# Performance work log

Measured on AMD Instinct MI355X. Metric: run time of the kernel, lower is better.

Reference implementation:

```python
import jax, jax.numpy as jnp
import numpy as np

N_NODES = 65536
N_GRAPHS = 32
NODES_PER_GRAPH = 2048
N_EDGES = 1048576
F_IN, H1, H2, OUT = 16, 64, 64, 12


def gcn_conv(x, src, dst, W, b, num_nodes):
    """PyG GCNConv: out = D^{-1/2} (A+I) D^{-1/2} X W + b."""
    loop = jnp.arange(num_nodes, dtype=src.dtype)
    s = jnp.concatenate([src, loop])  # sources incl. self-loops
    d = jnp.concatenate([dst, loop])  # targets incl. self-loops
    deg = jax.ops.segment_sum(jnp.ones_like(d, dtype=x.dtype), d, num_segments=num_nodes)
    dinv = jnp.where(deg > 0, jax.lax.rsqrt(deg), 0.0)
    norm = dinv[s] * dinv[d]  # [E+N]
    h = x @ W  # [N, H]
    msg = h[s] * norm[:, None]  # [E+N, H] -- dominant memory traffic
    return jax.ops.segment_sum(msg, d, num_segments=num_nodes) + b


def setup_inputs() -> dict:
    key = jax.random.key(0)
    k = jax.random.split(key, 8)
    x = jax.random.normal(k[0], (N_NODES, F_IN), dtype=jnp.float32)
    edge_index = jax.random.randint(k[1], (2, N_EDGES), 0, N_NODES, dtype=jnp.int32)
    batch = jnp.repeat(jnp.arange(N_GRAPHS, dtype=jnp.int32), NODES_PER_GRAPH)
    s1 = 1.0 / np.sqrt(F_IN)
    s2 = 1.0 / np.sqrt(H1)
    s3 = 1.0 / np.sqrt(H2 * NODES_PER_GRAPH)
    W1 = jax.random.uniform(k[2], (F_IN, H1), jnp.float32, -s1, s1)
    b1 = jnp.zeros((H1,), jnp.float32)
    W2 = jax.random.uniform(k[3], (H1, H2), jnp.float32, -s2, s2)
    b2 = jnp.zeros((H2,), jnp.float32)
    Wfc = jax.random.uniform(k[4], (H2 * NODES_PER_GRAPH, OUT), jnp.float32, -s3, s3)
    bfc = jax.random.uniform(k[5], (OUT,), jnp.float32, -s3, s3)
    return {"x": x, "edge_index": edge_index, "batch": batch,
            "W1": W1, "b1": b1, "W2": W2, "b2": b2, "Wfc": Wfc, "bfc": bfc}


def reference(x, edge_index, batch, W1, b1, W2, b2, Wfc, bfc):
    src, dst = edge_index[0], edge_index[1]
    h = gcn_conv(x, src, dst, W1, b1, N_NODES)
    h = jnp.tanh(h)  # act1 (dropout rate 0 -> identity)
    h = gcn_conv(h, src, dst, W2, b2, N_NODES)
    h = jnp.tanh(h)  # act2
    # batch is sorted with exactly NODES_PER_GRAPH nodes per graph, so the
    # per-graph masked concat is a reshape: [G, P*H2]
    h_concat = h.reshape(N_GRAPHS, NODES_PER_GRAPH * H2)
    return h_concat @ Wfc + bfc
```

## Files before the change

kernel.cpp:

```cpp
#include <hip/hip_runtime.h>
#include <hip/hip_fp16.h>

#define N_NODES 65536
#define N_EDGES 1048576
#define F_IN    16
#define H       64
#define N_GRAPHS 32
#define NPG     2048
#define OUT_F   12
#define KPG     (NPG * H)
#define CAP     4864
#define NPB     16


__global__ __launch_bounds__(256) void init_kernel(int* __restrict__ gCursor,
                                                   const float* __restrict__ bfc,
                                                   float* __restrict__ out) {
    int t = threadIdx.x;
    gCursor[t] = t * CAP;
    for (int i = t; i < N_GRAPHS * OUT_F; i += 256) out[i] = bfc[i % OUT_F];
}

__global__ __launch_bounds__(256) void binA_kernel(const int* __restrict__ src,
                                                   const int* __restrict__ dst,
                                                   int* __restrict__ gCursor,
                                                   unsigned int* __restrict__ binned) {
    __shared__ int hist[256];
    __shared__ int sc[256];
    __shared__ int bnd[256];
    __shared__ int lcur[256];
    __shared__ int blkBase[256];
    __shared__ unsigned int staged[4096];
    int t = threadIdx.x;
    hist[t] = 0; lcur[t] = 0;
    __syncthreads();
    int e0 = blockIdx.x * 4096;
    unsigned int rec[16];
#pragma unroll
    for (int i = 0; i < 16; i++) {
        int e = e0 + i * 256 + t;
        unsigned int s = (unsigned int)src[e];
        unsigned int d = (unsigned int)dst[e];
        rec[i] = s | (d << 16);
        atomicAdd(&hist[d >> 8], 1);
    }
    __syncthreads();
    int cnt = hist[t];
    if (cnt) blkBase[t] = atomicAdd(&gCursor[t], cnt);
    sc[t] = cnt;
    __syncthreads();
    for (int off = 1; off < 256; off <<= 1) {
        int v = (t >= off) ? sc[t - off] : 0;
        __syncthreads();
        sc[t] += v;
        __syncthreads();
    }
    bnd[t] = sc[t] - cnt;
    __syncthreads();
#pragma unroll
    for (int i = 0; i < 16; i++) {
        int b = rec[i] >> 24;
        int p = bnd[b] + atomicAdd(&lcur[b], 1);
        staged[p] = rec[i];
    }
    __syncthreads();
    for (int i = t; i < 4096; i += 256) {
        unsigned int r = staged[i];
        int b = r >> 24;
        binned[blkBase[b] + (i - bnd[b])] = r;
    }
}

__global__ __launch_bounds__(256) void binB_g1_kernel(const unsigned int* __restrict__ binned,
                                                      const int* __restrict__ gCursor,
                                                      const float* __restrict__ x,
                                                      int2* __restrict__ rowinfo,
                                                      unsigned short* __restrict__ nbr,
                                                      __half2* __restrict__ g1h) {
    __shared__ int hist[256];
    __shared__ int sc[256];
    __shared__ int off[256];
    __shared__ int cur[256];
    __shared__ unsigned short outS[8192];
    int b = blockIdx.x, t = threadIdx.x;
    int base = b * CAP;
    int cnt  = gCursor[b] - base;
    hist[t] = 0; cur[t] = 0;
    __syncthreads();
    for (int i = t; i < cnt; i += 256) {
        unsigned int r = binned[base + i];
        atomicAdd(&hist[(r >> 16) & 255], 1);
    }
    __syncthreads();
    int c = hist[t];
    sc[t] = c;
    __syncthreads();
    for (int o = 1; o < 256; o <<= 1) {
        int v = (t >= o) ? sc[t - o] : 0;
        __syncthreads();
        sc[t] += v;
        __syncthreads();
    }
    off[t] = sc[t] - c;
    int nd = (b << 8) + t;
    float dv = rsqrtf((float)(c + 1));
    rowinfo[nd] = make_int2(base + sc[t] - c, c);
    {
        const float4* xr = (const float4*)(x + (size_t)nd * F_IN);
        float4 x0 = xr[0], x1 = xr[1], x2 = xr[2], x3 = xr[3];
        __half2* gr = g1h + nd * 8;
        gr[0] = __floats2half2_rn(x0.x * dv, x0.y * dv);
        gr[1] = __floats2half2_rn(x0.z * dv, x0.w * dv);
        gr[2] = __floats2half2_rn(x1.x * dv, x1.y * dv);
        gr[3] = __floats2half2_rn(x1.z * dv, x1.w * dv);
        gr[4] = __floats2half2_rn(x2.x * dv, x2.y * dv);
        gr[5] = __floats2half2_rn(x2.z * dv, x2.w * dv);
        gr[6] = __floats2half2_rn(x3.x * dv, x3.y * dv);
        gr[7] = __floats2half2_rn(x3.z * dv, x3.w * dv);
    }
    __syncthreads();
    for (int i = t; i < cnt; i += 256) {
        unsigned int r = binned[base + i];
        int n = (r >> 16) & 255;
        int p = off[n] + atomicAdd(&cur[n], 1);
        outS[p] = (unsigned short)(r & 0xFFFF);
    }
    __syncthreads();
    for (int i = t; i < cnt; i += 256) nbr[base + i] = outS[i];
}

__device__ __forceinline__ void add8(float* acc, float4 q) {
    union { float4 f; __half2 h[4]; } u; u.f = q;
#pragma unroll
    for (int c = 0; c < 4; c++) {
        float2 p = __half22float2(u.h[c]);
        acc[2 * c]     += p.x;
        acc[2 * c + 1] += p.y;
    }
}
__device__ __forceinline__ void add4(float* acc, float2 q) {
    union { float2 f; __half2 h[2]; } u; u.f = q;
    float2 p0 = __half22float2(u.h[0]);
    float2 p1 = __half22float2(u.h[1]);
    acc[0] += p0.x; acc[1] += p0.y; acc[2] += p1.x; acc[3] += p1.y;
}

__global__ __launch_bounds__(256) void agg1_kernel(const __half2* __restrict__ g1h,
                                                   const int2* __restrict__ rowinfo,
                                                   const unsigned short* __restrict__ nbr,
                                                   float* __restrict__ a1) {
    const float2* g1v = (const float2*)g1h;
    int t    = threadIdx.x;
    int lane = t & 63;
    int w    = t >> 6;
    int f4   = lane & 3;
    int sub  = lane >> 2;
    int v    = blockIdx.x * NPB + w;
    int2 ri  = rowinfo[v];
    int nb   = (int)nbr[ri.x + lane];
#pragma unroll 1
    for (int it = 0; it < NPB / 4; ++it) {
        int vc = v;
        int r0 = ri.x, er = ri.y;
        int nbc = nb;
        float2 sq = g1v[(vc << 2) + f4];
        int s0 = sub, s1 = 16 + sub;
        int u0 = __shfl(nbc, s0 < er ? s0 : 0, 64);
        int u1 = __shfl(nbc, s1 < er ? s1 : 0, 64);
        float2 q0 = make_float2(0.f, 0.f), q1 = make_float2(0.f, 0.f);
        if (s0 < er) q0 = g1v[(u0 << 2) + f4];
        if (s1 < er) q1 = g1v[(u1 << 2) + f4];
        if (it < NPB / 4 - 1) ri = rowinfo[vc + 4];
        float acc[4] = {0.f, 0.f, 0.f, 0.f};
        add4(acc, q0);
        add4(acc, q1);
        int j = 32;
        for (; j + 32 <= er; j += 32) {
            int a0 = __shfl(nbc, j + sub, 64);
            int a1i = __shfl(nbc, j + 16 + sub, 64);
            float2 t0 = g1v[(a0 << 2) + f4];
            float2 t1 = g1v[(a1i << 2) + f4];
            add4(acc, t0);
            add4(acc, t1);
        }
        for (; j < er && j < 64; j += 16) {
            int idx = j + sub;
            int u = __shfl(nbc, idx < er ? idx : 0, 64);
            if (idx < er) {
                float2 q = g1v[(u << 2) + f4];
                add4(acc, q);
            }
        }
        for (int base = 64; base < er; base += 64) {
            int nbx = (int)nbr[r0 + base + lane];
            for (int jj = 0; jj < 64 && base + jj < er; jj += 16) {
                int idx = jj + sub;
                int u = __shfl(nbx, (base + idx) < er ? idx : 0, 64);
                if (base + idx < er) {
                    float2 q = g1v[(u << 2) + f4];
                    add4(acc, q);
                }
            }
        }
        if (it < NPB / 4 - 1) nb = (int)nbr[ri.x + lane];
#pragma unroll
        for (int i = 0; i < 4; i++) {
            acc[i] += __shfl_xor(acc[i], 4, 64);
            acc[i] += __shfl_xor(acc[i], 8, 64);
            acc[i] += __shfl_xor(acc[i], 16, 64);
            acc[i] += __shfl_xor(acc[i], 32, 64);
        }
        add4(acc, sq);
        float dv = rsqrtf((float)(er + 1));
        if (sub == 0) {
            float4* dp = (float4*)(a1 + ((size_t)vc << 4) + (f4 << 2));
            dp[0] = make_float4(dv * acc[0], dv * acc[1], dv * acc[2], dv * acc[3]);
        }
        v += 4;
    }
}

__global__ __launch_bounds__(256) void gemm1_kernel(const float* __restrict__ a1,
                                                    const int2* __restrict__ rowinfo,
                                                    const float* __restrict__ W1,
                                                    const float* __restrict__ b1,
                                                    __half* __restrict__ g2h) {
    __shared__ float Ws[F_IN * H];
    __shared__ float As[64 * F_IN];
    __shared__ float bs[H];
    __shared__ float degs[64];
    int t = threadIdx.x;
    for (int i = t; i < F_IN * H; i += 256) Ws[i] = W1[i];
    if (t < H) bs[t] = b1[t];
    int v0 = blockIdx.x * 64;
    if (t < 64) degs[t] = (float)(rowinfo[v0 + t].y + 1);
    {
        const float4* ap = (const float4*)(a1 + ((size_t)v0 << 4));
        ((float4*)As)[t] = ap[t];
    }
    __syncthreads();
    int lane = t & 63, w = t >> 6;
    float acc[16];
#pragma unroll
    for (int j = 0; j < 16; j++) acc[j] = bs[lane];
    const float* asBase = As + ((w << 4) * F_IN);
#pragma unroll
    for (int kc = 0; kc < F_IN / 4; ++kc) {
        int k0 = kc << 2;
        float w0 = Ws[(k0 + 0) * H + lane];
        float w1 = Ws[(k0 + 1) * H + lane];
        float w2 = Ws[(k0 + 2) * H + lane];
        float w3 = Ws[(k0 + 3) * H + lane];
#pragma unroll
        for (int j = 0; j < 16; ++j) {
            float4 aq = *(const float4*)(asBase + j * F_IN + k0);
            acc[j] += aq.x * w0 + aq.y * w1 + aq.z * w2 + aq.w * w3;
        }
    }
    int vw = v0 + (w << 4);
#pragma unroll
    for (int j = 0; j < 16; ++j) {
        float dv = rsqrtf(degs[(w << 4) + j]);
        g2h[((size_t)(vw + j) << 6) + lane] = __float2half(dv * tanhf(acc[j]));
    }
}

__global__ __launch_bounds__(256) void agg2_kernel(const __half2* __restrict__ g2h,
                                                   const int2* __restrict__ rowinfo,
                                                   const unsigned short* __restrict__ nbr,
                                                   float* __restrict__ a2) {
    const float4* g2v = (const float4*)g2h;
    int t    = threadIdx.x;
    int lane = t & 63;
    int w    = t >> 6;
    int f8   = lane & 7;
    int sub  = lane >> 3;
    int v    = blockIdx.x * NPB + w;
    int2 ri  = rowinfo[v];
    int nb   = (int)nbr[ri.x + lane];
#pragma unroll 1
    for (int it = 0; it < NPB / 4; ++it) {
        int vc = v;
        int r0 = ri.x, er = ri.y;
        int nbc = nb;
        float4 sq = g2v[(vc << 3) + f8];
        int s0 = sub, s1 = 8 + sub, s2 = 16 + sub, s3 = 24 + sub;
        int u0 = __shfl(nbc, s0 < er ? s0 : 0, 64);
        int u1 = __shfl(nbc, s1 < er ? s1 : 0, 64);
        int u2 = __shfl(nbc, s2 < er ? s2 : 0, 64);
        int u3 = __shfl(nbc, s3 < er ? s3 : 0, 64);
        float4 q0 = make_float4(0.f, 0.f, 0.f, 0.f);
        float4 q1 = q0, q2 = q0, q3 = q0;
        if (s0 < er) q0 = g2v[(u0 << 3) + f8];
        if (s1 < er) q1 = g2v[(u1 << 3) + f8];
        if (s2 < er) q2 = g2v[(u2 << 3) + f8];
        if (s3 < er) q3 = g2v[(u3 << 3) + f8];
        if (it < NPB / 4 - 1) ri = rowinfo[vc + 4];
        float acc[8] = {0.f, 0.f, 0.f, 0.f, 0.f, 0.f, 0.f, 0.f};
        add8(acc, q0);
        add8(acc, q1);
        add8(acc, q2);
        add8(acc, q3);
        int j = 32;
        for (; j + 16 <= er && j < 64; j += 16) {
            int a0 = __shfl(nbc, j + sub, 64);
            int a1i = __shfl(nbc, j + 8 + sub, 64);
            float4 t0 = g2v[(a0 << 3) + f8];
            float4 t1 = g2v[(a1i << 3) + f8];
            add8(acc, t0);
            add8(acc, t1);
        }
        for (; j < er && j < 64; j += 8) {
            int idx = j + sub;
            int u = __shfl(nbc, idx < er ? idx : 0, 64);
            if (idx < er) {
                float4 q = g2v[(u << 3) + f8];
                add8(acc, q);
            }
        }
        for (int base = 64; base < er; base += 64) {
            int nbx = (int)nbr[r0 + base + lane];
            for (int jj = 0; jj < 64 && base + jj < er; jj += 8) {
                int idx = jj + sub;
                int u = __shfl(nbx, (base + idx) < er ? idx : 0, 64);
                if (base + idx < er) {
                    float4 q = g2v[(u << 3) + f8];
                    add8(acc, q);
                }
            }
        }
        if (it < NPB / 4 - 1) nb = (int)nbr[ri.x + lane];
#pragma unroll
        for (int i = 0; i < 8; i++) {
            acc[i] += __shfl_xor(acc[i], 8, 64);
            acc[i] += __shfl_xor(acc[i], 16, 64);
            acc[i] += __shfl_xor(acc[i], 32, 64);
        }
        add8(acc, sq);
        float dv = rsqrtf((float)(er + 1));
#pragma unroll
        for (int i = 0; i < 8; i++) acc[i] *= dv;
        if (sub == 0) {
            float4* dp = (float4*)(a2 + ((size_t)vc << 6) + (f8 << 3));
            dp[0] = make_float4(acc[0], acc[1], acc[2], acc[3]);
            dp[1] = make_float4(acc[4], acc[5], acc[6], acc[7]);
        }
        v += 4;
    }
}

__global__ __launch_bounds__(256) void gemm2_fc_kernel(const float* __restrict__ a2,
                                                       const float* __restrict__ W2,
                                                       const float* __restrict__ b2,
                                                       const float* __restrict__ Wfc,
                                                       float* __restrict__ out) {
    __shared__ float Ws[H * H];
    __shared__ float As[64 * H];
    __shared__ float bs[H];
    __shared__ float red[4][OUT_F];
    int t = threadIdx.x;
    for (int i = t; i < H * H; i += 256) Ws[i] = W2[i];
    if (t < H) bs[t] = b2[t];
    {
        const float4* ap = (const float4*)(a2 + ((size_t)blockIdx.x << 12));
        float4* asp = (float4*)As;
#pragma unroll
        for (int i = 0; i < 4; i++) asp[i * 256 + t] = ap[i * 256 + t];
    }
    __syncthreads();
    int lane = t & 63, w = t >> 6;
    int v0 = blockIdx.x * 64 + (w << 4);
    int g  = blockIdx.x >> 5;
    float acc[16];
#pragma unroll
    for (int j = 0; j < 16; j++) acc[j] = bs[lane];
    const float* asBase = As + ((w << 4) * H);
#pragma unroll 2
    for (int kc = 0; kc < H / 4; ++kc) {
        int k0 = kc << 2;
        float w0 = Ws[(k0 + 0) * H + lane];
        float w1 = Ws[(k0 + 1) * H + lane];
        float w2 = Ws[(k0 + 2) * H + lane];
        float w3 = Ws[(k0 + 3) * H + lane];
#pragma unroll
        for (int j = 0; j < 16; ++j) {
            float4 aq = *(const float4*)(asBase + j * H + k0);
            acc[j] += aq.x * w0 + aq.y * w1 + aq.z * w2 + aq.w * w3;
        }
    }
    float pa[OUT_F];
#pragma unroll
    for (int j = 0; j < OUT_F; j++) pa[j] = 0.f;
#pragma unroll
    for (int j = 0; j < 16; ++j) {
        float hv = tanhf(acc[j]);
        int vl = (v0 + j) & (NPG - 1);
        const float4* wr = (const float4*)(Wfc + (size_t)(vl * H + lane) * OUT_F);
        float4 q0 = wr[0], q1 = wr[1], q2 = wr[2];
        pa[0]  += hv * q0.x;  pa[1]  += hv * q0.y;
        pa[2]  += hv * q0.z;  pa[3]  += hv * q0.w;
        pa[4]  += hv * q1.x;  pa[5]  += hv * q1.y;
        pa[6]  += hv * q1.z;  pa[7]  += hv * q1.w;
        pa[8]  += hv * q2.x;  pa[9]  += hv * q2.y;
        pa[10] += hv * q2.z;  pa[11] += hv * q2.w;
    }
#pragma unroll
    for (int j = 0; j < OUT_F; j++) {
        float vv = pa[j];
        vv += __shfl_xor(vv, 1, 64);  vv += __shfl_xor(vv, 2, 64);
        vv += __shfl_xor(vv, 4, 64);  vv += __shfl_xor(vv, 8, 64);
        vv += __shfl_xor(vv, 16, 64); vv += __shfl_xor(vv, 32, 64);
        pa[j] = vv;
    }
    if (lane == 0) {
#pragma unroll
        for (int j = 0; j < OUT_F; j++) red[w][j] = pa[j];
    }
    __syncthreads();
    if (t < OUT_F)
        atomicAdd(&out[g * OUT_F + t], red[0][t] + red[1][t] + red[2][t] + red[3][t]);
}

extern "C" void kernel_launch(void* const* d_in, const int* in_sizes, int n_in,
                              void* d_out, int out_size, void* d_ws, size_t ws_size,
                              hipStream_t stream) {
    const float* x    = (const float*)d_in[0];
    const int*   edge = (const int*)d_in[1];
    const int*   src  = edge;
    const int*   dst  = edge + N_EDGES;
    const float* W1  = (const float*)d_in[3];
    const float* b1  = (const float*)d_in[4];
    const float* W2  = (const float*)d_in[5];
    const float* b2  = (const float*)d_in[6];
    const float* Wfc = (const float*)d_in[7];
    const float* bfc = (const float*)d_in[8];
    float* out = (float*)d_out;

    char* p = (char*)d_ws;
    auto alloc = [&](size_t n) { char* r = p; p += (n + 255) & ~(size_t)255; return r; };
    int*   gCursor    = (int*)alloc(256 * 4);
    int2*  rowinfo    = (int2*)alloc((size_t)N_NODES * 8);
    unsigned short* nbr = (unsigned short*)alloc((size_t)256 * CAP * 2 + 256);
    __half* g1h       = (__half*)alloc((size_t)N_NODES * F_IN * 2);
    float* a1         = (float*)alloc((size_t)N_NODES * F_IN * 4);
    __half* g2h       = (__half*)alloc((size_t)N_NODES * H * 2);
    float* a2         = (float*)alloc((size_t)N_NODES * H * 4);
    unsigned int* binned = (unsigned int*)alloc((size_t)256 * CAP * 4);

    init_kernel<<<1, 256, 0, stream>>>(gCursor, bfc, out);
    binA_kernel<<<256, 256, 0, stream>>>(src, dst, gCursor, binned);
    binB_g1_kernel<<<256, 256, 0, stream>>>(binned, gCursor, x, rowinfo, nbr,
                                            (__half2*)g1h);
    agg1_kernel<<<N_NODES / NPB, 256, 0, stream>>>((const __half2*)g1h, rowinfo, nbr, a1);
    gemm1_kernel<<<N_NODES / 64, 256, 0, stream>>>(a1, rowinfo, W1, b1, g2h);
    agg2_kernel<<<N_NODES / NPB, 256, 0, stream>>>((const __half2*)g2h, rowinfo, nbr, a2);
    gemm2_fc_kernel<<<N_NODES / 64, 256, 0, stream>>>(a2, W2, b2, Wfc, out);
}
```

Before: 187.8 us.

## Fuse neighbor aggregation with dense GEMM stages via shared-memory staging

Merges agg1 with gemm1 and agg2 with gemm2+FC so each block aggregates 64 nodes into shared memory and then immediately runs the dense transform. This removes the a1/a2 intermediate global buffers, their write and read traffic, and two kernel launches. Grid size drops from 4096 to 1024 blocks, which lowers parallelism during the latency-bound gather phase. It also swaps tanhf for an exp-based fast tanh, which may lose some accuracy.

```diff
diff --git a/kernel.cpp b/kernel.cpp
--- a/kernel.cpp
+++ b/kernel.cpp
@@ -10,7 +10,6 @@
 #define OUT_F   12
 #define KPG     (NPG * H)
 #define CAP     4864
-#define NPB     16
 
 
 __global__ __launch_bounds__(256) void init_kernel(int* __restrict__ gCursor,
@@ -144,22 +143,35 @@
     float2 p1 = __half22float2(u.h[1]);
     acc[0] += p0.x; acc[1] += p0.y; acc[2] += p1.x; acc[3] += p1.y;
 }
-
-__global__ __launch_bounds__(256) void agg1_kernel(const __half2* __restrict__ g1h,
-                                                   const int2* __restrict__ rowinfo,
-                                                   const unsigned short* __restrict__ nbr,
-                                                   float* __restrict__ a1) {
+__device__ __forceinline__ float tanh_fast(float x) {
+    float e = __expf(2.f * x);
+    return 1.f - 2.f / (e + 1.f);
+}
+
+__global__ __launch_bounds__(256) void agg1_gemm1_kernel(const __half2* __restrict__ g1h,
+                                                         const int2* __restrict__ rowinfo,
+                                                         const unsigned short* __restrict__ nbr,
+                                                         const float* __restrict__ W1,
+                                                         const float* __restrict__ b1,
+                                                         __half* __restrict__ g2h) {
     const float2* g1v = (const float2*)g1h;
-    int t    = threadIdx.x;
+    __shared__ float Ws[F_IN * H];
+    __shared__ float As[64 * F_IN];
+    __shared__ float bs[H];
+    __shared__ float dvs[64];
+    int t = threadIdx.x;
+    for (int i = t; i < F_IN * H; i += 256) Ws[i] = W1[i];
+    if (t < H) bs[t] = b1[t];
     int lane = t & 63;
     int w    = t >> 6;
     int f4   = lane & 3;
     int sub  = lane >> 2;
-    int v    = blockIdx.x * NPB + w;
+    int v0   = blockIdx.x * 64;
+    int v    = v0 + w;
     int2 ri  = rowinfo[v];
     int nb   = (int)nbr[ri.x + lane];
 #pragma unroll 1
-    for (int it = 0; it < NPB / 4; ++it) {
+    for (int it = 0; it < 16; ++it) {
         int vc = v;
         int r0 = ri.x, er = ri.y;
         int nbc = nb;
@@ -170,7 +182,7 @@
         float2 q0 = make_float2(0.f, 0.f), q1 = make_float2(0.f, 0.f);
         if (s0 < er) q0 = g1v[(u0 << 2) + f4];
         if (s1 < er) q1 = g1v[(u1 << 2) + f4];
-        if (it < NPB / 4 - 1) ri = rowinfo[vc + 4];
+        if (it < 15) ri = rowinfo[vc + 4];
         float acc[4] = {0.f, 0.f, 0.f, 0.f};
         add4(acc, q0);
         add4(acc, q1);
@@ -186,23 +198,17 @@
         for (; j < er && j < 64; j += 16) {
             int idx = j + sub;
             int u = __shfl(nbc, idx < er ? idx : 0, 64);
-            if (idx < er) {
-                float2 q = g1v[(u << 2) + f4];
-                add4(acc, q);
-            }
+            if (idx < er) { float2 q = g1v[(u << 2) + f4]; add4(acc, q); }
         }
         for (int base = 64; base < er; base += 64) {
             int nbx = (int)nbr[r0 + base + lane];
             for (int jj = 0; jj < 64 && base + jj < er; jj += 16) {
                 int idx = jj + sub;
                 int u = __shfl(nbx, (base + idx) < er ? idx : 0, 64);
-                if (base + idx < er) {
-                    float2 q = g1v[(u << 2) + f4];
-                    add4(acc, q);
-                }
+                if (base + idx < er) { float2 q = g1v[(u << 2) + f4]; add4(acc, q); }
             }
         }
-        if (it < NPB / 4 - 1) nb = (int)nbr[ri.x + lane];
+        if (it < 15) nb = (int)nbr[ri.x + lane];
 #pragma unroll
         for (int i = 0; i < 4; i++) {
             acc[i] += __shfl_xor(acc[i], 4, 64);
@@ -212,37 +218,18 @@
         }
         add4(acc, sq);
         float dv = rsqrtf((float)(er + 1));
+        int nloc = (it << 2) + w;
         if (sub == 0) {
-            float4* dp = (float4*)(a1 + ((size_t)vc << 4) + (f4 << 2));
-            dp[0] = make_float4(dv * acc[0], dv * acc[1], dv * acc[2], dv * acc[3]);
+            *(float4*)&As[nloc * F_IN + (f4 << 2)] =
+                make_float4(dv * acc[0], dv * acc[1], dv * acc[2], dv * acc[3]);
+            if (f4 == 0) dvs[nloc] = dv;
         }
         v += 4;
     }
-}
-
-__global__ __launch_bounds__(256) void gemm1_kernel(const float* __restrict__ a1,
-                                                    const int2* __restrict__ rowinfo,
-                                                    const float* __restrict__ W1,
-                                                    const float* __restrict__ b1,
-                                                    __half* __restrict__ g2h) {
-    __shared__ float Ws[F_IN * H];
-    __shared__ float As[64 * F_IN];
-    __shared__ float bs[H];
-    __shared__ float degs[64];
-    int t = threadIdx.x;
-    for (int i = t; i < F_IN * H; i += 256) Ws[i] = W1[i];
-    if (t < H) bs[t] = b1[t];
-    int v0 = blockIdx.x * 64;
-    if (t < 64) degs[t] = (float)(rowinfo[v0 + t].y + 1);
-    {
-        const float4* ap = (const float4*)(a1 + ((size_t)v0 << 4));
-        ((float4*)As)[t] = ap[t];
-    }
-    __syncthreads();
-    int lane = t & 63, w = t >> 6;
-    float acc[16];
-#pragma unroll
-    for (int j = 0; j < 16; j++) acc[j] = bs[lane];
+    __syncthreads();
+    float acg[16];
+#pragma unroll
+    for (int j = 0; j < 16; j++) acg[j] = bs[lane];
     const float* asBase = As + ((w << 4) * F_IN);
 #pragma unroll
     for (int kc = 0; kc < F_IN / 4; ++kc) {
@@ -254,32 +241,42 @@
 #pragma unroll
         for (int j = 0; j < 16; ++j) {
             float4 aq = *(const float4*)(asBase + j * F_IN + k0);
-            acc[j] += aq.x * w0 + aq.y * w1 + aq.z * w2 + aq.w * w3;
+            acg[j] += aq.x * w0 + aq.y * w1 + aq.z * w2 + aq.w * w3;
         }
     }
     int vw = v0 + (w << 4);
 #pragma unroll
     for (int j = 0; j < 16; ++j) {
-        float dv = rsqrtf(degs[(w << 4) + j]);
-        g2h[((size_t)(vw + j) << 6) + lane] = __float2half(dv * tanhf(acc[j]));
-    }
-}
-
-__global__ __launch_bounds__(256) void agg2_kernel(const __half2* __restrict__ g2h,
-                                                   const int2* __restrict__ rowinfo,
-                                                   const unsigned short* __restrict__ nbr,
-                                                   float* __restrict__ a2) {
+        float dv = dvs[(w << 4) + j];
+        g2h[((size_t)(vw + j) << 6) + lane] = __float2half(dv * tanh_fast(acg[j]));
+    }
+}
+
+__global__ __launch_bounds__(256) void agg2_gemm2_fc_kernel(const __half2* __restrict__ g2h,
+                                                            const int2* __restrict__ rowinfo,
+                                                            const unsigned short* __restrict__ nbr,
+                                                            const float* __restrict__ W2,
+                                                            const float* __restrict__ b2,
+                                                            const float* __restrict__ Wfc,
+                                                            float* __restrict__ out) {
     const float4* g2v = (const float4*)g2h;
-    int t    = threadIdx.x;
+    __shared__ float Ws[H * H];
+    __shared__ float As[64 * H];
+    __shared__ float bs[H];
+    __shared__ float red[4][OUT_F];
+    int t = threadIdx.x;
+    for (int i = t; i < H * H; i += 256) Ws[i] = W2[i];
+    if (t < H) bs[t] = b2[t];
     int lane = t & 63;
     int w    = t >> 6;
     int f8   = lane & 7;
     int sub  = lane >> 3;
-    int v    = blockIdx.x * NPB + w;
+    int v0   = blockIdx.x * 64;
+    int v    = v0 + w;
     int2 ri  = rowinfo[v];
     int nb   = (int)nbr[ri.x + lane];
 #pragma unroll 1
-    for (int it = 0; it < NPB / 4; ++it) {
+    for (int it = 0; it < 16; ++it) {
         int vc = v;
         int r0 = ri.x, er = ri.y;
         int nbc = nb;
@@ -295,7 +292,7 @@
         if (s1 < er) q1 = g2v[(u1 << 3) + f8];
         if (s2 < er) q2 = g2v[(u2 << 3) + f8];
         if (s3 < er) q3 = g2v[(u3 << 3) + f8];
-        if (it < NPB / 4 - 1) ri = rowinfo[vc + 4];
+        if (it < 15) ri = rowinfo[vc + 4];
         float acc[8] = {0.f, 0.f, 0.f, 0.f, 0.f, 0.f, 0.f, 0.f};
         add8(acc, q0);
         add8(acc, q1);
@@ -313,23 +310,17 @@
         for (; j < er && j < 64; j += 8) {
             int idx = j + sub;
             int u = __shfl(nbc, idx < er ? idx : 0, 64);
-            if (idx < er) {
-                float4 q = g2v[(u << 3) + f8];
-                add8(acc, q);
-            }
+            if (idx < er) { float4 q = g2v[(u << 3) + f8]; add8(acc, q); }
         }
         for (int base = 64; base < er; base += 64) {
             int nbx = (int)nbr[r0 + base + lane];
             for (int jj = 0; jj < 64 && base + jj < er; jj += 8) {
                 int idx = jj + sub;
                 int u = __shfl(nbx, (base + idx) < er ? idx : 0, 64);
-                if (base + idx < er) {
-                    float4 q = g2v[(u << 3) + f8];
-                    add8(acc, q);
-                }
+                if (base + idx < er) { float4 q = g2v[(u << 3) + f8]; add8(acc, q); }
             }
         }
-        if (it < NPB / 4 - 1) nb = (int)nbr[ri.x + lane];
+        if (it < 15) nb = (int)nbr[ri.x + lane];
 #pragma unroll
         for (int i = 0; i < 8; i++) {
             acc[i] += __shfl_xor(acc[i], 8, 64);
@@ -338,42 +329,20 @@
         }
         add8(acc, sq);
         float dv = rsqrtf((float)(er + 1));
-#pragma unroll
-        for (int i = 0; i < 8; i++) acc[i] *= dv;
+        int nloc = (it << 2) + w;
         if (sub == 0) {
-            float4* dp = (float4*)(a2 + ((size_t)vc << 6) + (f8 << 3));
-            dp[0] = make_float4(acc[0], acc[1], acc[2], acc[3]);
-            dp[1] = make_float4(acc[4], acc[5], acc[6], acc[7]);
+            float* dp = &As[nloc * H + (f8 << 3)];
+            *(float4*)(dp)     = make_float4(dv * acc[0], dv * acc[1], dv * acc[2], dv * acc[3]);
+            *(float4*)(dp + 4) = make_float4(dv * acc[4], dv * acc[5], dv * acc[6], dv * acc[7]);
         }
         v += 4;
     }
-}
-
-__global__ __launch_bounds__(256) void gemm2_fc_kernel(const float* __restrict__ a2,
-                                                       const float* __restrict__ W2,
-                                                       const float* __restrict__ b2,
-                                                       const float* __restrict__ Wfc,
-                                                       float* __restrict__ out) {
-    __shared__ float Ws[H * H];
-    __shared__ float As[64 * H];
-    __shared__ float bs[H];
-    __shared__ float red[4][OUT_F];
-    int t = threadIdx.x;
-    for (int i = t; i < H * H; i += 256) Ws[i] = W2[i];
-    if (t < H) bs[t] = b2[t];
-    {
-        const float4* ap = (const float4*)(a2 + ((size_t)blockIdx.x << 12));
-        float4* asp = (float4*)As;
-#pragma unroll
-        for (int i = 0; i < 4; i++) asp[i * 256 + t] = ap[i * 256 + t];
-    }
-    __syncthreads();
-    int lane = t & 63, w = t >> 6;
-    int v0 = blockIdx.x * 64 + (w << 4);
+    __syncthreads();
+    int vw = v0 + (w << 4);
     int g  = blockIdx.x >> 5;
-    float acc[16];
-#pragma unroll
-    for (int j = 0; j < 16; j++) acc[j] = bs[lane];
+    float acg[16];
+#pragma unroll
+    for (int j = 0; j < 16; j++) acg[j] = bs[lane];
     const float* asBase = As + ((w << 4) * H);
 #pragma unroll 2
     for (int kc = 0; kc < H / 4; ++kc) {
@@ -385,7 +354,7 @@
 #pragma unroll
         for (int j = 0; j < 16; ++j) {
             float4 aq = *(const float4*)(asBase + j * H + k0);
-            acc[j] += aq.x * w0 + aq.y * w1 + aq.z * w2 + aq.w * w3;
+            acg[j] += aq.x * w0 + aq.y * w1 + aq.z * w2 + aq.w * w3;
         }
     }
     float pa[OUT_F];
@@ -393,8 +362,8 @@
     for (int j = 0; j < OUT_F; j++) pa[j] = 0.f;
 #pragma unroll
     for (int j = 0; j < 16; ++j) {
-        float hv = tanhf(acc[j]);
-        int vl = (v0 + j) & (NPG - 1);
+        float hv = tanh_fast(acg[j]);
+        int vl = (vw + j) & (NPG - 1);
         const float4* wr = (const float4*)(Wfc + (size_t)(vl * H + lane) * OUT_F);
         float4 q0 = wr[0], q1 = wr[1], q2 = wr[2];
         pa[0]  += hv * q0.x;  pa[1]  += hv * q0.y;
@@ -442,17 +411,15 @@
     int2*  rowinfo    = (int2*)alloc((size_t)N_NODES * 8);
     unsigned short* nbr = (unsigned short*)alloc((size_t)256 * CAP * 2 + 256);
     __half* g1h       = (__half*)alloc((size_t)N_NODES * F_IN * 2);
-    float* a1         = (float*)alloc((size_t)N_NODES * F_IN * 4);
     __half* g2h       = (__half*)alloc((size_t)N_NODES * H * 2);
-    float* a2         = (float*)alloc((size_t)N_NODES * H * 4);
     unsigned int* binned = (unsigned int*)alloc((size_t)256 * CAP * 4);
 
     init_kernel<<<1, 256, 0, stream>>>(gCursor, bfc, out);
     binA_kernel<<<256, 256, 0, stream>>>(src, dst, gCursor, binned);
     binB_g1_kernel<<<256, 256, 0, stream>>>(binned, gCursor, x, rowinfo, nbr,
                                             (__half2*)g1h);
-    agg1_kernel<<<N_NODES / NPB, 256, 0, stream>>>((const __half2*)g1h, rowinfo, nbr, a1);
-    gemm1_kernel<<<N_NODES / 64, 256, 0, stream>>>(a1, rowinfo, W1, b1, g2h);
-    agg2_kernel<<<N_NODES / NPB, 256, 0, stream>>>((const __half2*)g2h, rowinfo, nbr, a2);
-    gemm2_fc_kernel<<<N_NODES / 64, 256, 0, stream>>>(a2, W2, b2, Wfc, out);
-}
+    agg1_gemm1_kernel<<<N_NODES / 64, 256, 0, stream>>>((const __half2*)g1h, rowinfo, nbr,
+                                                        W1, b1, g2h);
+    agg2_gemm2_fc_kernel<<<N_NODES / 64, 256, 0, stream>>>((const __half2*)g2h, rowinfo, nbr,
+                                                           W2, b2, Wfc, out);
+}
```

Measured after the change: 204.0 us. 8.7% more time.
